# Optimization experiments

Hardware: AMD Instinct MI355X
Metric: run time of the kernel (lower is better)

The kernel has to match this reference:

```python
import jax, jax.numpy as jnp
import numpy as np

# --- model constants (cfg stand-ins) ---
V_TH = 1.0        # spike threshold
SURR_BETA = 0.2   # surrogate-gradient sigmoid slope
ALPHA_MEM = 0.9   # membrane leak
STP_DECAY = 0.95  # short-term plasticity recovery
STP_R = 0.3       # STP depression per spike
A_P = 0.01        # STDP potentiation amplitude (Abbott)
A_D = 0.012       # STDP depression amplitude (Abbott)

B, N, N_FF, D = 16, 2048, 512, 4  # batch, recurrent neurons, FF inputs, delays


def setup_inputs() -> dict:
    key = jax.random.key(0)
    ks = jax.random.split(key, 10)
    FF = jax.random.uniform(ks[0], (B, N_FF), dtype=jnp.float32)          # feedforward spikes/rates
    V = jax.random.normal(ks[1], (B, N), dtype=jnp.float32) * 0.5         # membrane potential
    th_adapt = jax.random.uniform(ks[2], (B, N), dtype=jnp.float32) * 0.2 # adaptive threshold (ALIF)
    Xbuf = (jax.random.uniform(ks[3], (D, B, N)) < 0.05).astype(jnp.float32)  # delayed spike buffer
    stp_state = jax.random.uniform(ks[4], (D, B, N), dtype=jnp.float32) * 0.1 - 0.05
    xbar_pre_int = jax.random.uniform(ks[5], (B, N), dtype=jnp.float32)   # presyn STDP trace (int)
    xbar_post = jax.random.uniform(ks[6], (B, N), dtype=jnp.float32)      # postsyn STDP trace
    xbar_pre_ff = jax.random.uniform(ks[7], (B, N_FF), dtype=jnp.float32) # presyn STDP trace (ff)
    W_int = jax.random.normal(ks[8], (N, N), dtype=jnp.float32) / np.sqrt(N)
    W_ff = jax.random.normal(ks[9], (N_FF, N), dtype=jnp.float32) / np.sqrt(N_FF)
    return dict(FF=FF, V=V, th_adapt=th_adapt, Xbuf=Xbuf, stp_state=stp_state,
                xbar_pre_int=xbar_pre_int, xbar_post=xbar_post, xbar_pre_ff=xbar_pre_ff,
                W_int=W_int, W_ff=W_ff)


def reference(FF, V, th_adapt, Xbuf, stp_state, xbar_pre_int, xbar_post, xbar_pre_ff, W_int, W_ff):
    # ALIFSpikes: spikes from membrane vs adaptive threshold (sigmoid surrogate),
    # delayed spikes Xd read from the circular buffer.
    X = jax.nn.sigmoid((V - (V_TH + th_adapt)) / SURR_BETA)          # [B,N]
    Xd = Xbuf                                                        # [D,B,N]

    # STP: per-presynaptic, per-delay short-term weight factor
    w_short = 1.0 + (stp_state * STP_DECAY - STP_R * Xd)             # [D,B,N]

    # Abbott STDP: pairwise pre/post trace modulation of base weights
    # w_long[b,i,j] = W[i,j] + A_P*xbar_pre[b,i]*X[b,j] - A_D*pre_spike[b,i]*xbar_post[b,j]
    w_long_int = (W_int[None]
                  + A_P * xbar_pre_int[:, :, None] * X[:, None, :]
                  - A_D * Xd[0][:, :, None] * xbar_post[:, None, :])  # [B,N,N]
    w_long_ff = (W_ff[None]
                 + A_P * xbar_pre_ff[:, :, None] * X[:, None, :]
                 - A_D * FF[:, :, None] * xbar_post[:, None, :])      # [B,N_FF,N]

    # DeltaSynapse: spike-gated, STP-modulated current accumulation
    current = (jnp.einsum('dbi,bij->bj', Xd * w_short, w_long_int)
               + jnp.einsum('bi,bij->bj', FF, w_long_ff))             # [B,N]

    # Membrane: leaky integration with reset-by-spike
    V_new = ALPHA_MEM * V * (1.0 - X) + current                      # [B,N]

    return jnp.stack([X, V_new])                                     # [2,B,N]
```

## Files before the change

### kernel.cpp

```cpp
#include <hip/hip_runtime.h>

#define BB 16
#define NN 2048
#define NFF 512
#define DD 4

#define ROWS 64
#define WR 16
#define YINT 32
#define YTOT 40
#define JC   128

__global__ __launch_bounds__(256) void snn_pre(
    const float* __restrict__ FF, const float* __restrict__ V,
    const float* __restrict__ th, const float* __restrict__ Xbuf,
    const float* __restrict__ stp, const float* __restrict__ xpre_int,
    const float* __restrict__ xpre_ff,
    float* __restrict__ out_X, float* __restrict__ T,
    float* __restrict__ scal_part)
{
    __shared__ float red[8];
    int idx = blockIdx.x * 256 + threadIdx.x;
    float p0, p1;
    if (idx < BB * NN) {
        float v = V[idx], t = th[idx];
        float x = 1.f / (1.f + expf(-(v - 1.f - t) * 5.f));
        out_X[idx] = x;
        float xd0 = Xbuf[idx];
        float acc = 0.f;
        #pragma unroll
        for (int d = 0; d < DD; ++d) {
            float xd = Xbuf[d * BB * NN + idx];
            float s  = stp[d * BB * NN + idx];
            acc += xd * (1.f + 0.95f * s - 0.3f * xd);
        }
        T[idx] = acc;
        p0 = acc * xpre_int[idx];
        p1 = acc * xd0;
    } else {
        int k = idx - BB * NN;
        float f = FF[k];
        p0 = f * xpre_ff[k];
        p1 = f * f;
    }
    #pragma unroll
    for (int o = 32; o; o >>= 1) { p0 += __shfl_xor(p0, o); p1 += __shfl_xor(p1, o); }
    int w = threadIdx.x >> 6;
    if ((threadIdx.x & 63) == 0) { red[w * 2] = p0; red[w * 2 + 1] = p1; }
    __syncthreads();
    if (threadIdx.x == 0) {
        scal_part[blockIdx.x * 2]     = red[0] + red[2] + red[4] + red[6];
        scal_part[blockIdx.x * 2 + 1] = red[1] + red[3] + red[5] + red[7];
    }
}

__global__ __launch_bounds__(256, 2) void snn_gemv(
    const float* __restrict__ Wint, const float* __restrict__ Wff,
    const float* __restrict__ T, const float* __restrict__ FF,
    float* __restrict__ part)
{
    __shared__ float c_lds[ROWS * BB];
    __shared__ float red[2 * 2 * BB * 64];
    int y = blockIdx.y;
    const float* Wm; const float* OP; int i0, opstride;
    if (y < YINT) { Wm = Wint; OP = T;  i0 = y * ROWS;          opstride = NN;  }
    else          { Wm = Wff;  OP = FF; i0 = (y - YINT) * ROWS; opstride = NFF; }

    int t = threadIdx.x;
    #pragma unroll
    for (int k = 0; k < ROWS * BB / 256; ++k) {
        int e = k * 256 + t;
        int row = e >> 4, b = e & 15;
        c_lds[e] = OP[b * opstride + i0 + row];
    }
    __syncthreads();

    int w = t >> 6, l = t & 63;
    int j0 = blockIdx.x * JC + l * 2;
    float2 acc[BB];
    #pragma unroll
    for (int b = 0; b < BB; ++b) acc[b] = make_float2(0.f, 0.f);

    const float* wp = Wm + (size_t)(i0 + w * WR) * NN + j0;
    float2 buf[WR];
    #pragma unroll
    for (int r = 0; r < WR; ++r) buf[r] = *(const float2*)(wp + (size_t)r * NN);

    #pragma unroll
    for (int r = 0; r < WR; ++r) {
        const float4* cb = (const float4*)&c_lds[(w * WR + r) * BB];
        float4 c0 = cb[0], c1 = cb[1], c2 = cb[2], c3 = cb[3];
        float2 wv = buf[r];
#define FMA2(b, cc) acc[b].x += (cc) * wv.x; acc[b].y += (cc) * wv.y;
        FMA2(0,  c0.x) FMA2(1,  c0.y) FMA2(2,  c0.z) FMA2(3,  c0.w)
        FMA2(4,  c1.x) FMA2(5,  c1.y) FMA2(6,  c1.z) FMA2(7,  c1.w)
        FMA2(8,  c2.x) FMA2(9,  c2.y) FMA2(10, c2.z) FMA2(11, c2.w)
        FMA2(12, c3.x) FMA2(13, c3.y) FMA2(14, c3.z) FMA2(15, c3.w)
#undef FMA2
    }

    if (w >= 2) {
        float* rb = &red[(w - 2) * 2 * BB * 64];
        #pragma unroll
        for (int b = 0; b < BB; ++b) {
            rb[(2 * b) * 64 + l]     = acc[b].x;
            rb[(2 * b + 1) * 64 + l] = acc[b].y;
        }
    }
    __syncthreads();
    if (w < 2) {
        const float* rb = &red[w * 2 * BB * 64];
        #pragma unroll
        for (int b = 0; b < BB; ++b) {
            acc[b].x += rb[(2 * b) * 64 + l];
            acc[b].y += rb[(2 * b + 1) * 64 + l];
        }
    }
    __syncthreads();
    if (w == 1) {
        #pragma unroll
        for (int b = 0; b < BB; ++b) {
            red[(2 * b) * 64 + l]     = acc[b].x;
            red[(2 * b + 1) * 64 + l] = acc[b].y;
        }
    }
    __syncthreads();
    if (w == 0) {
        float* pp = part + (size_t)y * (BB * NN) + j0;
        #pragma unroll
        for (int b = 0; b < BB; ++b) {
            acc[b].x += red[(2 * b) * 64 + l];
            acc[b].y += red[(2 * b + 1) * 64 + l];
            *(float2*)(pp + (size_t)b * NN) = acc[b];
        }
    }
}

__global__ __launch_bounds__(256) void snn_post(
    const float* __restrict__ V, const float* __restrict__ xpost,
    const float* __restrict__ part, const float* __restrict__ scal_part,
    const float* __restrict__ out_X, float* __restrict__ out_V)
{
    int idx = blockIdx.x * 256 + threadIdx.x;
    int b = idx >> 11;
    float c1 = 0.f, c2 = 0.f, c3 = 0.f, c4 = 0.f;
    #pragma unroll
    for (int k = 0; k < 8; ++k) {
        c1 += scal_part[(b * 8 + k) * 2];
        c2 += scal_part[(b * 8 + k) * 2 + 1];
    }
    #pragma unroll
    for (int k = 0; k < 2; ++k) {
        c3 += scal_part[(128 + b * 2 + k) * 2];
        c4 += scal_part[(128 + b * 2 + k) * 2 + 1];
    }
    float s = 0.f;
    #pragma unroll
    for (int yy = 0; yy < YTOT; ++yy) s += part[(size_t)yy * (BB * NN) + idx];
    float x = out_X[idx];
    float c = s + 0.01f * (c1 + c3) * x - 0.012f * (c2 + c4) * xpost[idx];
    out_V[idx] = 0.9f * V[idx] * (1.f - x) + c;
}

extern "C" void kernel_launch(void* const* d_in, const int* in_sizes, int n_in,
                              void* d_out, int out_size, void* d_ws, size_t ws_size,
                              hipStream_t stream) {
    const float* FF       = (const float*)d_in[0];
    const float* V        = (const float*)d_in[1];
    const float* th       = (const float*)d_in[2];
    const float* Xbuf     = (const float*)d_in[3];
    const float* stp      = (const float*)d_in[4];
    const float* xpre_int = (const float*)d_in[5];
    const float* xpost    = (const float*)d_in[6];
    const float* xpre_ff  = (const float*)d_in[7];
    const float* Wint     = (const float*)d_in[8];
    const float* Wff      = (const float*)d_in[9];
    float* out = (float*)d_out;
    float* ws  = (float*)d_ws;

    float* T    = ws;
    float* part = ws + BB * NN;
    float* sp   = ws + BB * NN + YTOT * BB * NN;

    snn_pre<<<(BB * NN + BB * NFF) / 256, 256, 0, stream>>>(
        FF, V, th, Xbuf, stp, xpre_int, xpre_ff, out, T, sp);

    snn_gemv<<<dim3(NN / JC, YTOT), 256, 0, stream>>>(
        Wint, Wff, T, FF, part);

    snn_post<<<BB * NN / 256, 256, 0, stream>>>(
        V, xpost, part, sp, out, out + BB * NN);
}
```

Measured before the change: 21.03 us.

## Fuse post-reduction into GEMV via last-block atomic counter per column tile

```diff
diff --git a/kernel.cpp b/kernel.cpp
--- a/kernel.cpp
+++ b/kernel.cpp
@@ -17,10 +17,11 @@
     const float* __restrict__ stp, const float* __restrict__ xpre_int,
     const float* __restrict__ xpre_ff,
     float* __restrict__ out_X, float* __restrict__ T,
-    float* __restrict__ scal_part)
+    float* __restrict__ scal_part, unsigned int* __restrict__ cnt)
 {
     __shared__ float red[8];
     int idx = blockIdx.x * 256 + threadIdx.x;
+    if (blockIdx.x == 0 && threadIdx.x < 16) cnt[threadIdx.x] = 0u;
     float p0, p1;
     if (idx < BB * NN) {
         float v = V[idx], t = th[idx];
@@ -57,10 +58,15 @@
 __global__ __launch_bounds__(256, 2) void snn_gemv(
     const float* __restrict__ Wint, const float* __restrict__ Wff,
     const float* __restrict__ T, const float* __restrict__ FF,
-    float* __restrict__ part)
+    const float* __restrict__ V, const float* __restrict__ xpost,
+    const float* __restrict__ scal_part, const float* __restrict__ out_X,
+    float* __restrict__ out_V, float* __restrict__ part,
+    unsigned int* __restrict__ cnt)
 {
     __shared__ float c_lds[ROWS * BB];
     __shared__ float red[2 * 2 * BB * 64];
+    __shared__ unsigned int tail_flag;
+    __shared__ float csum[4 * BB];
     int y = blockIdx.y;
     const float* Wm; const float* OP; int i0, opstride;
     if (y < YINT) { Wm = Wint; OP = T;  i0 = y * ROWS;          opstride = NN;  }
@@ -134,32 +140,45 @@
             *(float2*)(pp + (size_t)b * NN) = acc[b];
         }
     }
-}
-
-__global__ __launch_bounds__(256) void snn_post(
-    const float* __restrict__ V, const float* __restrict__ xpost,
-    const float* __restrict__ part, const float* __restrict__ scal_part,
-    const float* __restrict__ out_X, float* __restrict__ out_V)
-{
-    int idx = blockIdx.x * 256 + threadIdx.x;
-    int b = idx >> 11;
-    float c1 = 0.f, c2 = 0.f, c3 = 0.f, c4 = 0.f;
+
+    __syncthreads();
+    __threadfence();
+    if (t == 0) {
+        unsigned int old = atomicAdd(&cnt[blockIdx.x], 1u);
+        tail_flag = (old == YTOT - 1) ? 1u : 0u;
+    }
+    __syncthreads();
+    if (!tail_flag) return;
+    __threadfence();
+
+    if (t < 64) {
+        int c = t >> 4, b = t & 15;
+        float s = 0.f;
+        if (c < 2) {
+            #pragma unroll
+            for (int k = 0; k < 8; ++k) s += scal_part[(b * 8 + k) * 2 + c];
+        } else {
+            #pragma unroll
+            for (int k = 0; k < 2; ++k) s += scal_part[(128 + b * 2 + k) * 2 + (c - 2)];
+        }
+        csum[c * BB + b] = s;
+    }
+    __syncthreads();
+
+    int jj = blockIdx.x * JC + (t & 127);
+    int b0 = t >> 7;
     #pragma unroll
     for (int k = 0; k < 8; ++k) {
-        c1 += scal_part[(b * 8 + k) * 2];
-        c2 += scal_part[(b * 8 + k) * 2 + 1];
-    }
-    #pragma unroll
-    for (int k = 0; k < 2; ++k) {
-        c3 += scal_part[(128 + b * 2 + k) * 2];
-        c4 += scal_part[(128 + b * 2 + k) * 2 + 1];
-    }
-    float s = 0.f;
-    #pragma unroll
-    for (int yy = 0; yy < YTOT; ++yy) s += part[(size_t)yy * (BB * NN) + idx];
-    float x = out_X[idx];
-    float c = s + 0.01f * (c1 + c3) * x - 0.012f * (c2 + c4) * xpost[idx];
-    out_V[idx] = 0.9f * V[idx] * (1.f - x) + c;
+        int b = b0 + 2 * k;
+        int idx = b * NN + jj;
+        float s = 0.f;
+        #pragma unroll
+        for (int yy = 0; yy < YTOT; ++yy) s += part[(size_t)yy * (BB * NN) + idx];
+        float x = out_X[idx];
+        float c = s + 0.01f * (csum[0 * BB + b] + csum[2 * BB + b]) * x
+                    - 0.012f * (csum[1 * BB + b] + csum[3 * BB + b]) * xpost[idx];
+        out_V[idx] = 0.9f * V[idx] * (1.f - x) + c;
+    }
 }
 
 extern "C" void kernel_launch(void* const* d_in, const int* in_sizes, int n_in,
@@ -181,13 +200,11 @@
     float* T    = ws;
     float* part = ws + BB * NN;
     float* sp   = ws + BB * NN + YTOT * BB * NN;
+    unsigned int* cnt = (unsigned int*)(sp + 320);
 
     snn_pre<<<(BB * NN + BB * NFF) / 256, 256, 0, stream>>>(
-        FF, V, th, Xbuf, stp, xpre_int, xpre_ff, out, T, sp);
+        FF, V, th, Xbuf, stp, xpre_int, xpre_ff, out, T, sp, cnt);
 
     snn_gemv<<<dim3(NN / JC, YTOT), 256, 0, stream>>>(
-        Wint, Wff, T, FF, part);
-
-    snn_post<<<BB * NN / 256, 256, 0, stream>>>(
-        V, xpost, part, sp, out, out + BB * NN);
+        Wint, Wff, T, FF, V, xpost, sp, out, out + BB * NN, part, cnt);
 }
```

Result: slower. 75.00 us (+256.7%).
